# Optimization experiments

Measured on AMD Instinct MI355X. Metric: run time of the kernel, lower is better.

## Reference

```python
import jax, jax.numpy as jnp
import numpy as np

DIM = 1024
NHEADS = 16
HEAD_DIM = DIM // NHEADS


def setup_inputs() -> dict:
    key = jax.random.key(0)
    ks = jax.random.split(key, 11)
    B, S = 4, 2048
    scale = 1.0 / np.sqrt(DIM)
    inp = {
        "Q": jax.random.normal(ks[0], (B, S, DIM), jnp.float32),
        "K": jax.random.normal(ks[1], (B, S, DIM), jnp.float32),
        "V": jax.random.normal(ks[2], (B, S, DIM), jnp.float32),
        "Wq": jax.random.normal(ks[3], (DIM, DIM), jnp.float32) * scale,
        "bq": jnp.zeros((DIM,), jnp.float32),
        "Wk": jax.random.normal(ks[4], (DIM, DIM), jnp.float32) * scale,
        "bk": jnp.zeros((DIM,), jnp.float32),
        "Wv": jax.random.normal(ks[5], (DIM, DIM), jnp.float32) * scale,
        "bv": jnp.zeros((DIM,), jnp.float32),
        "Wo": jax.random.normal(ks[6], (DIM, DIM), jnp.float32) * scale,
        "bo": jnp.zeros((DIM,), jnp.float32),
    }
    return inp


def _split_heads(x):
    # [B, S, D] -> [B, H, S, hd]
    B, S, _ = x.shape
    return x.reshape(B, S, NHEADS, HEAD_DIM).transpose(0, 2, 1, 3)


def reference(Q, K, V, Wq, bq, Wk, bk, Wv, bv, Wo, bo):
    q = _split_heads(Q @ Wq + bq)  # [B,H,S,hd]
    k = _split_heads(K @ Wk + bk)
    v = _split_heads(V @ Wv + bv)
    scores = jnp.einsum("bhqd,bhkd->bhqk", q, k) / np.sqrt(HEAD_DIM)
    attn = jax.nn.softmax(scores, axis=-1)  # dropout p=0 -> identity
    out = jnp.einsum("bhqk,bhkd->bhqd", attn, v)  # [B,H,S,hd]
    B, H, S, hd = out.shape
    out = out.transpose(0, 2, 1, 3).reshape(B, S, H * hd)
    return out @ Wo + bo
```

## Files before the change

### kernel.cpp

```cpp
#include <hip/hip_runtime.h>
#include <hip/hip_bf16.h>
#include <math.h>

#define DIM     1024
#define NHEADS  16
#define HD      64
#define BATCH   4
#define SEQ     2048
#define M_TOT   (BATCH * SEQ)
#define QSCALE  0.180336880111f

using short8 = __attribute__((ext_vector_type(8))) short;
using bf16x4 = __attribute__((ext_vector_type(4))) short;
using f32x4  = __attribute__((ext_vector_type(4))) float;

__device__ inline unsigned short f2bf(float x) {
    __hip_bfloat16 h = __float2bfloat16(x);
    unsigned short u;
    __builtin_memcpy(&u, &h, sizeof(u));
    return u;
}
__device__ inline void st_o(float* p, float v)          { *p = v; }
__device__ inline void st_o(unsigned short* p, float v) { *p = f2bf(v); }

__device__ inline unsigned pk2bf(float a, float b) {
    unsigned ua, ub;
    __builtin_memcpy(&ua, &a, 4); __builtin_memcpy(&ub, &b, 4);
    ua += 0x8000u; ub += 0x8000u;
    return (ua >> 16) | (ub & 0xffff0000u);
}

__device__ inline void async16(const void* g, void* l) {
    __builtin_amdgcn_global_load_lds(
        (const __attribute__((address_space(1))) void*)g,
        (__attribute__((address_space(3))) void*)l, 16, 0, 0);
}

__global__ __launch_bounds__(256) void cvt3(
    const float* __restrict__ S0, const float* __restrict__ S1,
    const float* __restrict__ S2,
    unsigned short* __restrict__ D0, unsigned short* __restrict__ D1,
    unsigned short* __restrict__ D2)
{
    const float* src; unsigned short* dst;
    switch (blockIdx.y) {
        case 0:  src = S0; dst = D0; break;
        case 1:  src = S1; dst = D1; break;
        default: src = S2; dst = D2; break;
    }
    const size_t i = ((size_t)blockIdx.x * 256 + threadIdx.x) * 16;
    unsigned short tmp[16];
    #pragma unroll
    for (int p = 0; p < 4; ++p) {
        const float4 v = *(const float4*)(src + i + p * 4);
        tmp[p * 4 + 0] = f2bf(v.x); tmp[p * 4 + 1] = f2bf(v.y);
        tmp[p * 4 + 2] = f2bf(v.z); tmp[p * 4 + 3] = f2bf(v.w);
    }
    *(short8*)(dst + i)     = *(short8*)&tmp[0];
    *(short8*)(dst + i + 8) = *(short8*)&tmp[8];
}

__global__ __launch_bounds__(256) void wcvt4(
    const float* __restrict__ W0, const float* __restrict__ W1,
    const float* __restrict__ W2, const float* __restrict__ W3,
    unsigned short* __restrict__ T0, unsigned short* __restrict__ T1,
    unsigned short* __restrict__ T2, unsigned short* __restrict__ T3)
{
    const float* W; unsigned short* Wt;
    switch (blockIdx.z) {
        case 0:  W = W0; Wt = T0; break;
        case 1:  W = W1; Wt = T1; break;
        case 2:  W = W2; Wt = T2; break;
        default: W = W3; Wt = T3; break;
    }
    __shared__ unsigned short tile[32][33];
    const int t = threadIdx.x;
    const int tx = t & 31, ty = t >> 5;
    const int n0 = blockIdx.x * 32, k0 = blockIdx.y * 32;
    #pragma unroll
    for (int i = 0; i < 4; ++i) {
        const int kk = ty + i * 8;
        tile[kk][tx] = f2bf(W[(size_t)(k0 + kk) * DIM + n0 + tx]);
    }
    __syncthreads();
    #pragma unroll
    for (int i = 0; i < 4; ++i) {
        const int nn = ty + i * 8;
        Wt[(size_t)(n0 + nn) * DIM + k0 + tx] = tile[tx][nn];
    }
}

template <typename TY, bool TRANSV>
__device__ __forceinline__ void gemm_body(
    const unsigned short* A, const unsigned short* Wt,
    const float* bias, TY* Y, float scale,
    unsigned short* As, unsigned short* Bs)
{
    const int t = threadIdx.x;
    const int lane = t & 63, wv = t >> 6;
    const int wm = wv >> 1, wn = wv & 1;
    const int l16 = lane & 15, lq = lane >> 4;

    const unsigned lin = blockIdx.y * 8 + blockIdx.x;
    const unsigned wg  = (lin & 7) * 64 + (lin >> 3);
    const int m0 = (int)(wg >> 3) * 128, n0 = (int)(wg & 7) * 128;

    const int lrow = lane >> 2;
    const int lcol = (lane & 3) * 8;

    f32x4 acc[4][4] = {};

    #pragma unroll
    for (int c = 0; c < 2; ++c) {
        const int ci  = wv * 2 + c;
        const int row = ci * 16 + lrow;
        async16(A  + (size_t)(m0 + row) * DIM + lcol, &As[ci * 512]);
        async16(Wt + (size_t)(n0 + row) * DIM + lcol, &Bs[ci * 512]);
    }
    __syncthreads();

    int cur = 0;
    for (int k0 = 0; k0 < DIM; k0 += 32) {
        if (k0 + 32 < DIM) {
            unsigned short* Ad = As + (cur ^ 1) * 4096;
            unsigned short* Bd = Bs + (cur ^ 1) * 4096;
            #pragma unroll
            for (int c = 0; c < 2; ++c) {
                const int ci  = wv * 2 + c;
                const int row = ci * 16 + lrow;
                async16(A  + (size_t)(m0 + row) * DIM + k0 + 32 + lcol, Ad + ci * 512);
                async16(Wt + (size_t)(n0 + row) * DIM + k0 + 32 + lcol, Bd + ci * 512);
            }
        }
        const unsigned short* Ac = As + cur * 4096;
        const unsigned short* Bc = Bs + cur * 4096;

        short8 af[4], bfr[4];
        #pragma unroll
        for (int mi = 0; mi < 4; ++mi)
            af[mi] = *(const short8*)&Ac[(wm * 64 + mi * 16 + l16) * 32 + lq * 8];
        #pragma unroll
        for (int nj = 0; nj < 4; ++nj)
            bfr[nj] = *(const short8*)&Bc[(wn * 64 + nj * 16 + l16) * 32 + lq * 8];
        #pragma unroll
        for (int mi = 0; mi < 4; ++mi)
            #pragma unroll
            for (int nj = 0; nj < 4; ++nj)
                acc[mi][nj] = __builtin_amdgcn_mfma_f32_16x16x32_bf16(
                    af[mi], bfr[nj], acc[mi][nj], 0, 0, 0);

        __syncthreads();
        cur ^= 1;
    }

    #pragma unroll
    for (int mi = 0; mi < 4; ++mi)
        #pragma unroll
        for (int nj = 0; nj < 4; ++nj) {
            const int row = m0 + wm * 64 + mi * 16 + lq * 4;
            const int col = n0 + wn * 64 + nj * 16 + l16;
            const float bb = bias[col];
            if constexpr (TRANSV) {
                unsigned short o[4];
                #pragma unroll
                for (int r = 0; r < 4; ++r)
                    o[r] = f2bf((acc[mi][nj][r] + bb) * scale);
                const int bb_ = row >> 11, ss = row & (SEQ - 1);
                unsigned short* dst = (unsigned short*)Y +
                    ((size_t)(bb_ * NHEADS + (col >> 6)) * HD + (col & 63)) * SEQ + ss;
                *(bf16x4*)dst = *(const bf16x4*)o;
            } else {
                #pragma unroll
                for (int r = 0; r < 4; ++r)
                    st_o(&Y[(size_t)(row + r) * DIM + col],
                         (acc[mi][nj][r] + bb) * scale);
            }
        }
}

template <typename TY, bool TRANSV = false>
__global__ __launch_bounds__(256) void gemm_a16(
    const unsigned short* __restrict__ A, const unsigned short* __restrict__ Wt,
    const float* __restrict__ bias, TY* __restrict__ Y, float scale)
{
    __shared__ unsigned short As[2 * 128 * 32];
    __shared__ unsigned short Bs[2 * 128 * 32];
    gemm_body<TY, TRANSV>(A, Wt, bias, Y, scale, As, Bs);
}

__global__ __launch_bounds__(256) void gemm_qkv(
    const unsigned short* Av, const unsigned short* Wtv, const float* bv_,
    unsigned short* Yv,
    const unsigned short* Aq, const unsigned short* Wtq, const float* bq_,
    unsigned short* Yq,
    const unsigned short* Ak, const unsigned short* Wtk, const float* bk_,
    unsigned short* Yk)
{
    __shared__ unsigned short As[2 * 128 * 32];
    __shared__ unsigned short Bs[2 * 128 * 32];
    const int z = blockIdx.z;
    if (z == 0)
        gemm_body<unsigned short, true >(Av, Wtv, bv_, Yv, 1.0f,   As, Bs);
    else if (z == 1)
        gemm_body<unsigned short, false>(Aq, Wtq, bq_, Yq, QSCALE, As, Bs);
    else
        gemm_body<unsigned short, false>(Ak, Wtk, bk_, Yk, 1.0f,   As, Bs);
}

__global__ __launch_bounds__(256) void attn_mfma(
    const unsigned short* __restrict__ qbuf, const unsigned short* __restrict__ kbuf,
    const unsigned short* __restrict__ vtb, unsigned short* __restrict__ ctx)
{
    __shared__ unsigned short Kls[2 * 64 * 64];
    __shared__ unsigned short Vls[2 * 64 * 64];
    __shared__ unsigned short Qls[64 * 64];

    const int t = threadIdx.x;
    const int lane = t & 63, wv = t >> 6;
    const int l16 = lane & 15, lq = lane >> 4;
    const int l7 = l16 & 7;
    const int lqh = lq >> 1, lql4 = (lq & 1) * 4;

    const unsigned lin  = (blockIdx.z * gridDim.y + blockIdx.y) * gridDim.x + blockIdx.x;
    const unsigned xcd  = lin & 7, slot = lin >> 3;
    const unsigned bh   = ((slot >> 5) << 3) | xcd;
    const int b = (int)(bh >> 4), h = (int)(bh & 15);
    const int q0 = (int)(slot & 31) * 64;

    const size_t base  = ((size_t)b * SEQ) * DIM + h * HD;
    const size_t vbase = ((size_t)(b * NHEADS + h)) * HD * SEQ;

    const int rl   = lane >> 3;
    const int gcol = ((lane & 7) ^ rl) << 3;

    {
        const int r = t >> 2, c = (t & 3) * 16;
        const int g0 = c >> 3, rx = r & 7;
        const unsigned short* src = qbuf + base + (size_t)(q0 + r) * DIM + c;
        *(short8*)&Qls[r * 64 + ((g0 ^ rx) << 3)]       = *(const short8*)src;
        *(short8*)&Qls[r * 64 + (((g0 + 1) ^ rx) << 3)] = *(const short8*)(src + 8);
    }
    const int qrow = wv * 16 + l16;
    const short8 qf0 = *(const short8*)&Qls[qrow * 64 + ((lq ^ l7) << 3)];
    const short8 qf1 = *(const short8*)&Qls[qrow * 64 + (((4 + lq) ^ l7) << 3)];

    float l_acc = 0.f;
    f32x4 O[4] = {};

    #pragma unroll
    for (int c = 0; c < 2; ++c) {
        const int ci = wv * 2 + c;
        async16(kbuf + base + (size_t)(ci * 8 + rl) * DIM + gcol, Kls + ci * 512);
        async16(vtb + vbase + (size_t)(ci * 8 + rl) * SEQ + gcol, Vls + ci * 512);
    }
    __syncthreads();

    int cur = 0;
    for (int s0 = 0; s0 < SEQ; s0 += 64) {
        const unsigned short* Kc = Kls + cur * 4096;
        const unsigned short* Vc = Vls + cur * 4096;

        if (s0 + 64 < SEQ) {
            unsigned short* Kd = Kls + (cur ^ 1) * 4096;
            unsigned short* Vd = Vls + (cur ^ 1) * 4096;
            #pragma unroll
            for (int c = 0; c < 2; ++c) {
                const int ci = wv * 2 + c;
                async16(kbuf + base + (size_t)(s0 + 64 + ci * 8 + rl) * DIM + gcol,
                        Kd + ci * 512);
                async16(vtb + vbase + (size_t)(ci * 8 + rl) * SEQ + s0 + 64 + gcol,
                        Vd + ci * 512);
            }
        }

        __builtin_amdgcn_s_setprio(1);

        f32x4 sa[4] = {};
        #pragma unroll
        for (int ti = 0; ti < 4; ++ti) {
            const int rr = ti * 16 + l16;
            const short8 kf0 = *(const short8*)(Kc + rr * 64 + ((lq ^ l7) << 3));
            const short8 kf1 = *(const short8*)(Kc + rr * 64 + (((4 + lq) ^ l7) << 3));
            sa[ti] = __builtin_amdgcn_mfma_f32_16x16x32_bf16(kf0, qf0, sa[ti], 0, 0, 0);
            sa[ti] = __builtin_amdgcn_mfma_f32_16x16x32_bf16(kf1, qf1, sa[ti], 0, 0, 0);
        }

        #pragma unroll
        for (int ti = 0; ti < 4; ++ti) {
            const float v0 = __builtin_amdgcn_exp2f(sa[ti][0]);
            const float v1 = __builtin_amdgcn_exp2f(sa[ti][1]);
            const float v2 = __builtin_amdgcn_exp2f(sa[ti][2]);
            const float v3 = __builtin_amdgcn_exp2f(sa[ti][3]);
            l_acc += (v0 + v1) + (v2 + v3);
            unsigned pw[2] = { pk2bf(v0, v1), pk2bf(v2, v3) };
            bf16x4 pa;
            __builtin_memcpy(&pa, pw, 8);
            #pragma unroll
            for (int dt = 0; dt < 4; ++dt) {
                const int vr = dt * 16 + l16;
                const bf16x4 vb = *(const bf16x4*)(
                    Vc + vr * 64 + (((2 * ti + lqh) ^ l7) << 3) + lql4);
                O[dt] = __builtin_amdgcn_mfma_f32_16x16x16bf16_1k(pa, vb, O[dt], 0, 0, 0);
            }
        }

        __builtin_amdgcn_s_setprio(0);

        __syncthreads();
        cur ^= 1;
    }

    l_acc += __shfl_xor(l_acc, 16);
    l_acc += __shfl_xor(l_acc, 32);

    unsigned short (*Ol)[72] = (unsigned short(*)[72])Kls;
    #pragma unroll
    for (int r = 0; r < 4; ++r) {
        const float inv = 1.0f / __shfl(l_acc, lq * 4 + r);
        const int orow = wv * 16 + lq * 4 + r;
        #pragma unroll
        for (int dt = 0; dt < 4; ++dt)
            Ol[orow][dt * 16 + l16] = f2bf(O[dt][r] * inv);
    }
    __syncthreads();
    {
        const int r = t >> 2, c = (t & 3) * 16;
        unsigned short* dst = ctx + base + (size_t)(q0 + r) * DIM + c;
        *(short8*)dst       = *(const short8*)&Ol[r][c];
        *(short8*)(dst + 8) = *(const short8*)&Ol[r][c + 8];
    }
}

extern "C" void kernel_launch(void* const* d_in, const int* in_sizes, int n_in,
                              void* d_out, int out_size, void* d_ws, size_t ws_size,
                              hipStream_t stream) {
    const float* Q  = (const float*)d_in[0];
    const float* K  = (const float*)d_in[1];
    const float* V  = (const float*)d_in[2];
    const float* Wq = (const float*)d_in[3];
    const float* bq = (const float*)d_in[4];
    const float* Wk = (const float*)d_in[5];
    const float* bk = (const float*)d_in[6];
    const float* Wv = (const float*)d_in[7];
    const float* bv = (const float*)d_in[8];
    const float* Wo = (const float*)d_in[9];
    const float* bo = (const float*)d_in[10];
    float* out = (float*)d_out;

    const size_t eW = (size_t)DIM * DIM;
    const size_t eB = (size_t)M_TOT * DIM;
    unsigned short* p   = (unsigned short*)d_ws;
    unsigned short* wtq = p; p += eW;
    unsigned short* wtk = p; p += eW;
    unsigned short* wtv = p; p += eW;
    unsigned short* wto = p; p += eW;
    unsigned short* bufA = p; p += eB;
    unsigned short* bufB = p; p += eB;
    unsigned short* bufC = p; p += eB;
    unsigned short* bufD = p; p += eB;
    unsigned short* bufE = p;
    unsigned short* qfs = (unsigned short*)out;

    wcvt4<<<dim3(32, 32, 4), 256, 0, stream>>>(Wq, Wk, Wv, Wo, wtq, wtk, wtv, wto);

    const int cvt_blocks = (int)(eB / (256 * 16));
    cvt3<<<dim3(cvt_blocks, 3), 256, 0, stream>>>(V, Q, K, bufA, bufC, bufB);

    gemm_qkv<<<dim3(DIM / 128, M_TOT / 128, 3), 256, 0, stream>>>(
        bufA, wtv, bv, bufE,
        bufC, wtq, bq, qfs,
        bufB, wtk, bk, bufD);

    attn_mfma<<<dim3(SEQ / 64, NHEADS, BATCH), 256, 0, stream>>>(qfs, bufD, bufE, bufA);

    gemm_a16<float><<<dim3(DIM / 128, M_TOT / 128), 256, 0, stream>>>(
        bufA, wto, bo, out, 1.0f);
}
```

Measured before the change: 356.1 us.

## Use 128-query attention blocks with 8 waves sharing each K/V tile

The attention kernel now runs 512 threads per block covering 128 query rows, so each K/V tile staged in LDS is reused by twice as many waves. Each wave issues one async K and one async V load instead of two of each, which halves global K/V traffic per query. The grid is halved and the XCD remap is adjusted to match. The cost is fewer, larger blocks with more LDS per block, which could reduce occupancy. The setprio region is also split around the QK and PV phases.

```diff
diff --git a/kernel.cpp b/kernel.cpp
--- a/kernel.cpp
+++ b/kernel.cpp
@@ -207,13 +207,11 @@
         gemm_body<unsigned short, false>(Ak, Wtk, bk_, Yk, 1.0f,   As, Bs);
 }
 
-__global__ __launch_bounds__(256) void attn_mfma(
+__global__ __launch_bounds__(512) void attn_mfma(
     const unsigned short* __restrict__ qbuf, const unsigned short* __restrict__ kbuf,
     const unsigned short* __restrict__ vtb, unsigned short* __restrict__ ctx)
 {
-    __shared__ unsigned short Kls[2 * 64 * 64];
-    __shared__ unsigned short Vls[2 * 64 * 64];
-    __shared__ unsigned short Qls[64 * 64];
+    __shared__ unsigned short lds[24576];
 
     const int t = threadIdx.x;
     const int lane = t & 63, wv = t >> 6;
@@ -223,9 +221,9 @@
 
     const unsigned lin  = (blockIdx.z * gridDim.y + blockIdx.y) * gridDim.x + blockIdx.x;
     const unsigned xcd  = lin & 7, slot = lin >> 3;
-    const unsigned bh   = ((slot >> 5) << 3) | xcd;
+    const unsigned bh   = ((slot >> 4) << 3) | xcd;
     const int b = (int)(bh >> 4), h = (int)(bh & 15);
-    const int q0 = (int)(slot & 31) * 64;
+    const int q0 = (int)(slot & 15) * 128;
 
     const size_t base  = ((size_t)b * SEQ) * DIM + h * HD;
     const size_t vbase = ((size_t)(b * NHEADS + h)) * HD * SEQ;
@@ -237,45 +235,34 @@
         const int r = t >> 2, c = (t & 3) * 16;
         const int g0 = c >> 3, rx = r & 7;
         const unsigned short* src = qbuf + base + (size_t)(q0 + r) * DIM + c;
-        *(short8*)&Qls[r * 64 + ((g0 ^ rx) << 3)]       = *(const short8*)src;
-        *(short8*)&Qls[r * 64 + (((g0 + 1) ^ rx) << 3)] = *(const short8*)(src + 8);
+        *(short8*)&lds[16384 + r * 64 + ((g0 ^ rx) << 3)]       = *(const short8*)src;
+        *(short8*)&lds[16384 + r * 64 + (((g0 + 1) ^ rx) << 3)] = *(const short8*)(src + 8);
     }
     const int qrow = wv * 16 + l16;
-    const short8 qf0 = *(const short8*)&Qls[qrow * 64 + ((lq ^ l7) << 3)];
-    const short8 qf1 = *(const short8*)&Qls[qrow * 64 + (((4 + lq) ^ l7) << 3)];
+    const short8 qf0 = *(const short8*)&lds[16384 + qrow * 64 + ((lq ^ l7) << 3)];
+    const short8 qf1 = *(const short8*)&lds[16384 + qrow * 64 + (((4 + lq) ^ l7) << 3)];
 
     float l_acc = 0.f;
     f32x4 O[4] = {};
 
-    #pragma unroll
-    for (int c = 0; c < 2; ++c) {
-        const int ci = wv * 2 + c;
-        async16(kbuf + base + (size_t)(ci * 8 + rl) * DIM + gcol, Kls + ci * 512);
-        async16(vtb + vbase + (size_t)(ci * 8 + rl) * SEQ + gcol, Vls + ci * 512);
-    }
+    async16(kbuf + base + (size_t)(wv * 8 + rl) * DIM + gcol, lds + wv * 512);
+    async16(vtb + vbase + (size_t)(wv * 8 + rl) * SEQ + gcol, lds + 8192 + wv * 512);
     __syncthreads();
 
     int cur = 0;
     for (int s0 = 0; s0 < SEQ; s0 += 64) {
-        const unsigned short* Kc = Kls + cur * 4096;
-        const unsigned short* Vc = Vls + cur * 4096;
+        const unsigned short* Kc = lds + cur * 4096;
+        const unsigned short* Vc = lds + 8192 + cur * 4096;
 
         if (s0 + 64 < SEQ) {
-            unsigned short* Kd = Kls + (cur ^ 1) * 4096;
-            unsigned short* Vd = Vls + (cur ^ 1) * 4096;
-            #pragma unroll
-            for (int c = 0; c < 2; ++c) {
-                const int ci = wv * 2 + c;
-                async16(kbuf + base + (size_t)(s0 + 64 + ci * 8 + rl) * DIM + gcol,
-                        Kd + ci * 512);
-                async16(vtb + vbase + (size_t)(ci * 8 + rl) * SEQ + s0 + 64 + gcol,
-                        Vd + ci * 512);
-            }
-        }
-
+            async16(kbuf + base + (size_t)(s0 + 64 + wv * 8 + rl) * DIM + gcol,
+                    lds + (cur ^ 1) * 4096 + wv * 512);
+            async16(vtb + vbase + (size_t)(wv * 8 + rl) * SEQ + s0 + 64 + gcol,
+                    lds + 8192 + (cur ^ 1) * 4096 + wv * 512);
+        }
+
+        f32x4 sa[4] = {};
         __builtin_amdgcn_s_setprio(1);
-
-        f32x4 sa[4] = {};
         #pragma unroll
         for (int ti = 0; ti < 4; ++ti) {
             const int rr = ti * 16 + l16;
@@ -284,7 +271,9 @@
             sa[ti] = __builtin_amdgcn_mfma_f32_16x16x32_bf16(kf0, qf0, sa[ti], 0, 0, 0);
             sa[ti] = __builtin_amdgcn_mfma_f32_16x16x32_bf16(kf1, qf1, sa[ti], 0, 0, 0);
         }
-
+        __builtin_amdgcn_s_setprio(0);
+
+        __builtin_amdgcn_s_setprio(1);
         #pragma unroll
         for (int ti = 0; ti < 4; ++ti) {
             const float v0 = __builtin_amdgcn_exp2f(sa[ti][0]);
@@ -303,7 +292,6 @@
                 O[dt] = __builtin_amdgcn_mfma_f32_16x16x16bf16_1k(pa, vb, O[dt], 0, 0, 0);
             }
         }
-
         __builtin_amdgcn_s_setprio(0);
 
         __syncthreads();
@@ -313,7 +301,7 @@
     l_acc += __shfl_xor(l_acc, 16);
     l_acc += __shfl_xor(l_acc, 32);
 
-    unsigned short (*Ol)[72] = (unsigned short(*)[72])Kls;
+    unsigned short (*Ol)[72] = (unsigned short(*)[72])lds;
     #pragma unroll
     for (int r = 0; r < 4; ++r) {
         const float inv = 1.0f / __shfl(l_acc, lq * 4 + r);
@@ -371,7 +359,7 @@
         bufC, wtq, bq, qfs,
         bufB, wtk, bk, bufD);
 
-    attn_mfma<<<dim3(SEQ / 64, NHEADS, BATCH), 256, 0, stream>>>(qfs, bufD, bufE, bufA);
+    attn_mfma<<<dim3(SEQ / 128, NHEADS, BATCH), 512, 0, stream>>>(qfs, bufD, bufE, bufA);
 
     gemm_a16<float><<<dim3(DIM / 128, M_TOT / 128), 256, 0, stream>>>(
         bufA, wto, bo, out, 1.0f);
```

Result: no change. 361.1 us (+1.4%).
